# Performance work log

Hardware: AMD Instinct MI355X
Metric: run time of the kernel (lower is better)

The kernel has to match this reference:

```python
import jax, jax.numpy as jnp
import numpy as np

N = 8192
C = 256


def setup_inputs() -> dict:
    key = jax.random.key(0)
    k_x, k_wr, k_br, k_wc, k_bc = jax.random.split(key, 5)
    scale = 1.0 / np.sqrt(C)
    return {
        "x": jax.random.normal(k_x, (N, C), dtype=jnp.float32),
        "w_reduce": jax.random.uniform(k_wr, (C, C), dtype=jnp.float32, minval=-scale, maxval=scale),
        "b_reduce": jax.random.uniform(k_br, (C,), dtype=jnp.float32, minval=-scale, maxval=scale),
        "w_contr": jax.random.uniform(k_wc, (1, C), dtype=jnp.float32, minval=-scale, maxval=scale),
        "b_contr": jax.random.uniform(k_bc, (1,), dtype=jnp.float32, minval=-scale, maxval=scale),
    }


def reference(x, w_reduce, b_reduce, w_contr, b_contr):
    # Original math: y_ij = reduce(x_i + x_j); z_ij = sigmoid(contr(y_ij));
    # out_i = mean_j y_ij * z_ij.
    # Since reduce/contr are affine, decompose without the [N,N,C] tensor:
    #   y_ij = r_i + r_j + b_reduce,        r = x @ Wr^T
    #   contr(y_ij) = s_i + s_j + c0,       s = r . wc, c0 = b_reduce . wc + bc
    n = x.shape[0]
    r = x @ w_reduce.T                                   # [N, C]
    wc = w_contr[0]                                      # [C]
    s = r @ wc                                           # [N]
    c0 = b_reduce @ wc + b_contr[0]                      # scalar
    Z = jax.nn.sigmoid(s[:, None] + s[None, :] + c0)     # [N, N] pairwise gate
    m = jnp.mean(Z, axis=1, keepdims=True)               # [N, 1]
    # mean_j (r_i + r_j + b) * z_ij = (r_i + b) * m_i + (Z @ r)_i / N
    out = (r + b_reduce) * m + (Z @ r) / n               # [N, C]
    return out
```

## Files before the change

kernel.cpp:

```cpp
#include <hip/hip_runtime.h>
#include <hip/hip_bf16.h>
#include <stdint.h>

#define NN 8192
#define CC 256
#define NSPLIT 8
#define JR (NN / NSPLIT)
#define NITER (JR / 32)

typedef float f32x4 __attribute__((ext_vector_type(4)));
typedef float f32x2 __attribute__((ext_vector_type(2)));
typedef short s16x8 __attribute__((ext_vector_type(8)));

#define LOG2E 1.4426950408889634f

#define OFF_WT  0
#define OFF_R   (OFF_WT + CC*CC)
#define OFF_S2  (OFF_R + NN*CC)
#define OFF_C0  (OFF_S2 + NN)
#define OFF_SS  (OFF_C0 + 16)
#define OFF_SP  (OFF_SS + NSPLIT*NN)
#define OFF_V   (OFF_SP + 4*NN)
#define OFF_RB  (OFF_V + (NSPLIT*NN*CC)/2)

__global__ __launch_bounds__(256) void k_prep(const float* __restrict__ w,
                                              const float* __restrict__ br,
                                              const float* __restrict__ wcv,
                                              const float* __restrict__ bc,
                                              float* __restrict__ ws) {
  int k = blockIdx.x, c = threadIdx.x;
  ws[OFF_WT + k * CC + c] = w[c * CC + k];
  if (blockIdx.x == 0 && threadIdx.x < 64) {
    int lane = threadIdx.x;
    f32x4 b4 = *(const f32x4*)&br[lane * 4];
    f32x4 w4 = *(const f32x4*)&wcv[lane * 4];
    float d = b4[0]*w4[0] + b4[1]*w4[1] + b4[2]*w4[2] + b4[3]*w4[3];
    #pragma unroll
    for (int m = 32; m >= 1; m >>= 1) d += __shfl_xor(d, m, 64);
    if (lane == 0) { ws[OFF_C0] = d + bc[0]; ws[OFF_C0 + 1] = (d + bc[0]) * LOG2E; }
  }
}

__global__ __launch_bounds__(256) void k_r(const float* __restrict__ x,
                                           const float* __restrict__ wcv,
                                           float* __restrict__ ws) {
  __shared__ float xs[64][260];
  int bi = blockIdx.x;
  int rowblk = bi >> 2, colblk = bi & 3;
  int tid = threadIdx.x;
  int i0 = rowblk * 64;
  for (int t = tid; t < 64 * 64; t += 256) {
    int rr = t >> 6, c4 = t & 63;
    *(f32x4*)&xs[rr][c4 * 4] = *(const f32x4*)&x[(i0 + rr) * CC + c4 * 4];
  }
  __syncthreads();
  int tx = tid & 15, ty = tid >> 4;
  int cbase = colblk * 64 + tx * 4;
  int r0 = ty * 4;
  float acc[4][4] = {};
  const float* wt = ws + OFF_WT;
  for (int k = 0; k < CC; k += 2) {
    f32x4 wv0 = *(const f32x4*)&wt[k * CC + cbase];
    f32x4 wv1 = *(const f32x4*)&wt[(k + 1) * CC + cbase];
    f32x2 xv[4];
    #pragma unroll
    for (int rr = 0; rr < 4; rr++) xv[rr] = *(const f32x2*)&xs[r0 + rr][k];
    #pragma unroll
    for (int rr = 0; rr < 4; rr++)
      #pragma unroll
      for (int cc = 0; cc < 4; cc++)
        acc[rr][cc] = fmaf(xv[rr][1], wv1[cc], fmaf(xv[rr][0], wv0[cc], acc[rr][cc]));
  }
  #pragma unroll
  for (int rr = 0; rr < 4; rr++) {
    f32x4 o = {acc[rr][0], acc[rr][1], acc[rr][2], acc[rr][3]};
    *(f32x4*)&ws[OFF_R + (size_t)(i0 + r0 + rr) * CC + cbase] = o;
  }
  unsigned long long* rb64 = (unsigned long long*)(ws + OFF_RB);
  int j0r = i0 + r0;
  #pragma unroll
  for (int cc = 0; cc < 4; cc++) {
    int c = cbase + cc;
    unsigned long long v = 0;
    #pragma unroll
    for (int rr = 0; rr < 4; rr++) {
      unsigned u = __float_as_uint(acc[rr][cc]);
      u = (u + 0x7fffu + ((u >> 16) & 1u)) >> 16;
      v |= (unsigned long long)u << (16 * rr);
    }
    int us = (((j0r >> 5) * 16 + (c >> 4)) * 64 + (((j0r >> 3) & 3) * 16 + (c & 15))) * 8 + (j0r & 7);
    rb64[us >> 2] = v;
  }
  f32x4 wc4 = *(const f32x4*)&wcv[cbase];
  float sd[4];
  #pragma unroll
  for (int rr = 0; rr < 4; rr++) {
    sd[rr] = acc[rr][0]*wc4[0] + acc[rr][1]*wc4[1] + acc[rr][2]*wc4[2] + acc[rr][3]*wc4[3];
    #pragma unroll
    for (int m = 1; m < 16; m <<= 1) sd[rr] += __shfl_xor(sd[rr], m, 64);
  }
  if (tx == 0) {
    #pragma unroll
    for (int rr = 0; rr < 4; rr++)
      ws[OFF_SP + colblk * NN + j0r + rr] = sd[rr];
  }
}

__global__ __launch_bounds__(256) void k_s2(float* __restrict__ ws) {
  int row = blockIdx.x * 256 + threadIdx.x;
  float s = ws[OFF_SP + row] + ws[OFF_SP + NN + row]
          + ws[OFF_SP + 2 * NN + row] + ws[OFF_SP + 3 * NN + row];
  ws[OFF_S2 + row] = s * LOG2E;
}


#define STAGE(BUF, IT) { \
  const char* gb_ = rbase + (size_t)(IT) * 16384 + w * 1024 + l * 16; \
  _Pragma("unroll") \
  for (int q_ = 0; q_ < 4; q_++) \
    __builtin_amdgcn_global_load_lds( \
      (const __attribute__((address_space(1))) void*)(gb_ + q_ * 4096), \
      (__attribute__((address_space(3))) void*)&ldsb[(BUF) * 16384 + w * 1024 + q_ * 4096], \
      16, 0, 0); }

#define WAITBAR4 { asm volatile("s_waitcnt vmcnt(4)" ::: "memory"); \
  __builtin_amdgcn_s_barrier(); \
  __builtin_amdgcn_sched_barrier(0); }

#define WAITBAR0 { asm volatile("s_waitcnt vmcnt(0)" ::: "memory"); \
  __builtin_amdgcn_s_barrier(); \
  __builtin_amdgcn_sched_barrier(0); }

#define SB0 __builtin_amdgcn_sched_barrier(0);

#define SIGMOID(IT, AFA, AFB) { \
  f32x4 sj0_ = *(const f32x4*)&s2l[(IT) * 32 + g * 8]; \
  f32x4 sj1_ = *(const f32x4*)&s2l[(IT) * 32 + g * 8 + 4]; \
  _Pragma("unroll") \
  for (int t_ = 0; t_ < 8; t_++) { \
    float sj_ = (t_ < 4) ? sj0_[t_] : sj1_[t_ - 4]; \
    float eA_, eB_; \
    asm("v_exp_f32 %0, %1" : "=v"(eA_) : "v"(negaA - sj_)); \
    asm("v_exp_f32 %0, %1" : "=v"(eB_) : "v"(negaB - sj_)); \
    float zA_ = __builtin_amdgcn_rcpf(1.0f + eA_); \
    float zB_ = __builtin_amdgcn_rcpf(1.0f + eB_); \
    (AFA)[t_] = (short)(__float_as_uint(zA_) >> 16); \
    (AFB)[t_] = (short)(__float_as_uint(zB_) >> 16); } }

#define BLOAD(BF, LP) { \
  _Pragma("unroll") \
  for (int ct_ = 0; ct_ < 16; ct_++) \
    BF[ct_] = *(const s16x8*)((LP) + ct_ * 1024 + l * 16); }

#define MFMA_APPLY(AFA, AFB, BF) { \
  _Pragma("unroll") \
  for (int ct_ = 0; ct_ < 16; ct_++) { \
    accA[ct_] = __builtin_amdgcn_mfma_f32_16x16x32_bf16(AFA, BF[ct_], accA[ct_], 0, 0, 0); \
    accB[ct_] = __builtin_amdgcn_mfma_f32_16x16x32_bf16(AFB, BF[ct_], accB[ct_], 0, 0, 0); } \
  acc1A = __builtin_amdgcn_mfma_f32_16x16x32_bf16(AFA, ones, acc1A, 0, 0, 0); \
  acc1B = __builtin_amdgcn_mfma_f32_16x16x32_bf16(AFB, ones, acc1B, 0, 0, 0); }

__global__ __launch_bounds__(256, 2) void k_main(float* __restrict__ ws) {
  __shared__ char ldsb[3 * 16384];
  __shared__ float s2l[1024];
  int blk = blockIdx.x;
  int rt = blk >> 3, h = blk & 7;
  int tid = threadIdx.x;
  int w = tid >> 6, l = tid & 63;
  int lr = l & 15, g = l >> 4;
  int iw = rt * 128 + w * 32;
  float c02 = ws[OFF_C0 + 1];
  float negaA = -(ws[OFF_S2 + iw + lr] + c02);
  float negaB = -(ws[OFF_S2 + iw + 16 + lr] + c02);

  const float* s2p = ws + OFF_S2 + h * JR;
  *(f32x4*)&s2l[tid * 4] = *(const f32x4*)(s2p + tid * 4);
  __syncthreads();

  f32x4 accA[16], accB[16], acc1A, acc1B;
  #pragma unroll
  for (int i = 0; i < 16; i++) { accA[i] = (f32x4)(0.f); accB[i] = (f32x4)(0.f); }
  acc1A = (f32x4)(0.f); acc1B = (f32x4)(0.f);
  s16x8 ones;
  #pragma unroll
  for (int t = 0; t < 8; t++) ones[t] = (short)0x3F80;

  const char* rbase = (const char*)(ws + OFF_RB) + (size_t)h * (JR * CC * 2);

  STAGE(0, 0);
  STAGE(1, 1);
  s16x8 afA0, afB0, afA1, afB1;
  s16x8 bf[16];
  SIGMOID(0, afA0, afB0);

  int sA = 0;
  #pragma unroll 1
  for (int J = 0; J < NITER - 2; J += 2) {
    int sB = sA + 1; if (sB == 3) sB = 0;
    int sC = sB + 1; if (sC == 3) sC = 0;

    WAITBAR4;
    STAGE(sC, J + 2);
    SB0;
    BLOAD(bf, ldsb + sA * 16384);
    SB0;
    SIGMOID(J + 1, afA1, afB1);
    MFMA_APPLY(afA0, afB0, bf);

    WAITBAR4;
    STAGE(sA, J + 3);
    SB0;
    BLOAD(bf, ldsb + sB * 16384);
    SB0;
    SIGMOID(J + 2, afA0, afB0);
    MFMA_APPLY(afA1, afB1, bf);

    sA = sC;
  }
  {
    int sB = sA + 1; if (sB == 3) sB = 0;
    WAITBAR4;
    BLOAD(bf, ldsb + sA * 16384);
    SB0;
    SIGMOID(NITER - 1, afA1, afB1);
    MFMA_APPLY(afA0, afB0, bf);
    WAITBAR0;
    BLOAD(bf, ldsb + sB * 16384);
    MFMA_APPLY(afA1, afB1, bf);
  }

  if (lr == 0) {
    #pragma unroll
    for (int q = 0; q < 4; q++) {
      ws[OFF_SS + h * NN + iw + g * 4 + q] = acc1A[q];
      ws[OFF_SS + h * NN + iw + 16 + g * 4 + q] = acc1B[q];
    }
  }
  unsigned short* Vb = (unsigned short*)(ws + OFF_V);
  size_t vbase = (size_t)h * (NN * CC);
  #pragma unroll
  for (int ct = 0; ct < 16; ct++) {
    #pragma unroll
    for (int q = 0; q < 4; q++) {
      unsigned uA = __float_as_uint(accA[ct][q]);
      uA = (uA + 0x7fffu + ((uA >> 16) & 1u)) >> 16;
      Vb[vbase + (size_t)(iw + g * 4 + q) * CC + ct * 16 + lr] = (unsigned short)uA;
      unsigned uB = __float_as_uint(accB[ct][q]);
      uB = (uB + 0x7fffu + ((uB >> 16) & 1u)) >> 16;
      Vb[vbase + (size_t)(iw + 16 + g * 4 + q) * CC + ct * 16 + lr] = (unsigned short)uB;
    }
  }
}

__global__ __launch_bounds__(256) void k_epi(const float* __restrict__ br,
                                             const float* __restrict__ ws,
                                             float* __restrict__ out) {
  int idx = blockIdx.x * 256 + threadIdx.x;
  int i = idx >> 5, c8 = (idx & 31) * 8;
  float S = 0.f;
  #pragma unroll
  for (int p = 0; p < NSPLIT; p++) S += ws[OFF_SS + p * NN + i];
  float m = S * (1.0f / NN);
  float v[8] = {};
  const unsigned short* Vb = (const unsigned short*)(ws + OFF_V);
  #pragma unroll
  for (int p = 0; p < NSPLIT; p++) {
    s16x8 pv = *(const s16x8*)&Vb[(size_t)p * (NN * CC) + (size_t)i * CC + c8];
    #pragma unroll
    for (int t = 0; t < 8; t++)
      v[t] += __uint_as_float(((unsigned)(unsigned short)pv[t]) << 16);
  }
  f32x4 r0 = *(const f32x4*)&ws[OFF_R + (size_t)i * CC + c8];
  f32x4 r1 = *(const f32x4*)&ws[OFF_R + (size_t)i * CC + c8 + 4];
  f32x4 b0 = *(const f32x4*)&br[c8];
  f32x4 b1 = *(const f32x4*)&br[c8 + 4];
  f32x4 o0, o1;
  #pragma unroll
  for (int t = 0; t < 4; t++) {
    o0[t] = (r0[t] + b0[t]) * m + v[t] * (1.0f / NN);
    o1[t] = (r1[t] + b1[t]) * m + v[t + 4] * (1.0f / NN);
  }
  *(f32x4*)&out[(size_t)i * CC + c8] = o0;
  *(f32x4*)&out[(size_t)i * CC + c8 + 4] = o1;
}

extern "C" void kernel_launch(void* const* d_in, const int* in_sizes, int n_in,
                              void* d_out, int out_size, void* d_ws, size_t ws_size,
                              hipStream_t stream) {
  const float* x  = (const float*)d_in[0];
  const float* w  = (const float*)d_in[1];
  const float* br = (const float*)d_in[2];
  const float* wc = (const float*)d_in[3];
  const float* bc = (const float*)d_in[4];
  float* ws = (float*)d_ws;
  float* out = (float*)d_out;
  (void)in_sizes; (void)n_in; (void)out_size; (void)ws_size;

  k_prep<<<256, 256, 0, stream>>>(w, br, wc, bc, ws);
  k_r<<<512, 256, 0, stream>>>(x, wc, ws);
  k_s2<<<32, 256, 0, stream>>>(ws);
  k_main<<<512, 256, 0, stream>>>(ws);
  k_epi<<<1024, 256, 0, stream>>>(br, ws, out);
}
```

Baseline: 84.64 us.

## Switch pairwise gate GEMM from bf16 to fp8 MFMA with fp8-packed operands

```diff
diff --git a/kernel.cpp b/kernel.cpp
--- a/kernel.cpp
+++ b/kernel.cpp
@@ -76,20 +76,16 @@
     f32x4 o = {acc[rr][0], acc[rr][1], acc[rr][2], acc[rr][3]};
     *(f32x4*)&ws[OFF_R + (size_t)(i0 + r0 + rr) * CC + cbase] = o;
   }
-  unsigned long long* rb64 = (unsigned long long*)(ws + OFF_RB);
+  unsigned* rb32 = (unsigned*)(ws + OFF_RB);
   int j0r = i0 + r0;
   #pragma unroll
   for (int cc = 0; cc < 4; cc++) {
     int c = cbase + cc;
-    unsigned long long v = 0;
-    #pragma unroll
-    for (int rr = 0; rr < 4; rr++) {
-      unsigned u = __float_as_uint(acc[rr][cc]);
-      u = (u + 0x7fffu + ((u >> 16) & 1u)) >> 16;
-      v |= (unsigned long long)u << (16 * rr);
-    }
+    unsigned pk = 0;
+    pk = __builtin_amdgcn_cvt_pk_fp8_f32(acc[0][cc], acc[1][cc], (int)pk, false);
+    pk = __builtin_amdgcn_cvt_pk_fp8_f32(acc[2][cc], acc[3][cc], (int)pk, true);
     int us = (((j0r >> 5) * 16 + (c >> 4)) * 64 + (((j0r >> 3) & 3) * 16 + (c & 15))) * 8 + (j0r & 7);
-    rb64[us >> 2] = v;
+    rb32[us >> 2] = pk;
   }
   f32x4 wc4 = *(const f32x4*)&wcv[cbase];
   float sd[4];
@@ -115,15 +111,15 @@
 
 
 #define STAGE(BUF, IT) { \
-  const char* gb_ = rbase + (size_t)(IT) * 16384 + w * 1024 + l * 16; \
+  const char* gb_ = rbase + (size_t)(IT) * 8192 + w * 1024 + l * 16; \
   _Pragma("unroll") \
-  for (int q_ = 0; q_ < 4; q_++) \
+  for (int q_ = 0; q_ < 2; q_++) \
     __builtin_amdgcn_global_load_lds( \
       (const __attribute__((address_space(1))) void*)(gb_ + q_ * 4096), \
-      (__attribute__((address_space(3))) void*)&ldsb[(BUF) * 16384 + w * 1024 + q_ * 4096], \
+      (__attribute__((address_space(3))) void*)&ldsb[(BUF) * 8192 + w * 1024 + q_ * 4096], \
       16, 0, 0); }
 
-#define WAITBAR4 { asm volatile("s_waitcnt vmcnt(4)" ::: "memory"); \
+#define WAITBAR2 { asm volatile("s_waitcnt vmcnt(2)" ::: "memory"); \
   __builtin_amdgcn_s_barrier(); \
   __builtin_amdgcn_sched_barrier(0); }
 
@@ -136,32 +132,42 @@
 #define SIGMOID(IT, AFA, AFB) { \
   f32x4 sj0_ = *(const f32x4*)&s2l[(IT) * 32 + g * 8]; \
   f32x4 sj1_ = *(const f32x4*)&s2l[(IT) * 32 + g * 8 + 4]; \
+  float zA_[8], zB_[8]; \
   _Pragma("unroll") \
   for (int t_ = 0; t_ < 8; t_++) { \
     float sj_ = (t_ < 4) ? sj0_[t_] : sj1_[t_ - 4]; \
     float eA_, eB_; \
     asm("v_exp_f32 %0, %1" : "=v"(eA_) : "v"(negaA - sj_)); \
     asm("v_exp_f32 %0, %1" : "=v"(eB_) : "v"(negaB - sj_)); \
-    float zA_ = __builtin_amdgcn_rcpf(1.0f + eA_); \
-    float zB_ = __builtin_amdgcn_rcpf(1.0f + eB_); \
-    (AFA)[t_] = (short)(__float_as_uint(zA_) >> 16); \
-    (AFB)[t_] = (short)(__float_as_uint(zB_) >> 16); } }
+    zA_[t_] = __builtin_amdgcn_rcpf(1.0f + eA_); \
+    zB_[t_] = __builtin_amdgcn_rcpf(1.0f + eB_); } \
+  unsigned loA_ = 0, hiA_ = 0, loB_ = 0, hiB_ = 0; \
+  loA_ = __builtin_amdgcn_cvt_pk_fp8_f32(zA_[0], zA_[1], (int)loA_, false); \
+  loA_ = __builtin_amdgcn_cvt_pk_fp8_f32(zA_[2], zA_[3], (int)loA_, true); \
+  hiA_ = __builtin_amdgcn_cvt_pk_fp8_f32(zA_[4], zA_[5], (int)hiA_, false); \
+  hiA_ = __builtin_amdgcn_cvt_pk_fp8_f32(zA_[6], zA_[7], (int)hiA_, true); \
+  loB_ = __builtin_amdgcn_cvt_pk_fp8_f32(zB_[0], zB_[1], (int)loB_, false); \
+  loB_ = __builtin_amdgcn_cvt_pk_fp8_f32(zB_[2], zB_[3], (int)loB_, true); \
+  hiB_ = __builtin_amdgcn_cvt_pk_fp8_f32(zB_[4], zB_[5], (int)hiB_, false); \
+  hiB_ = __builtin_amdgcn_cvt_pk_fp8_f32(zB_[6], zB_[7], (int)hiB_, true); \
+  AFA = (long)(((unsigned long long)hiA_ << 32) | loA_); \
+  AFB = (long)(((unsigned long long)hiB_ << 32) | loB_); }
 
 #define BLOAD(BF, LP) { \
   _Pragma("unroll") \
   for (int ct_ = 0; ct_ < 16; ct_++) \
-    BF[ct_] = *(const s16x8*)((LP) + ct_ * 1024 + l * 16); }
+    BF[ct_] = *(const long*)((LP) + ct_ * 512 + l * 8); }
 
 #define MFMA_APPLY(AFA, AFB, BF) { \
   _Pragma("unroll") \
   for (int ct_ = 0; ct_ < 16; ct_++) { \
-    accA[ct_] = __builtin_amdgcn_mfma_f32_16x16x32_bf16(AFA, BF[ct_], accA[ct_], 0, 0, 0); \
-    accB[ct_] = __builtin_amdgcn_mfma_f32_16x16x32_bf16(AFB, BF[ct_], accB[ct_], 0, 0, 0); } \
-  acc1A = __builtin_amdgcn_mfma_f32_16x16x32_bf16(AFA, ones, acc1A, 0, 0, 0); \
-  acc1B = __builtin_amdgcn_mfma_f32_16x16x32_bf16(AFB, ones, acc1B, 0, 0, 0); }
+    accA[ct_] = __builtin_amdgcn_mfma_f32_16x16x32_fp8_fp8(AFA, BF[ct_], accA[ct_], 0, 0, 0); \
+    accB[ct_] = __builtin_amdgcn_mfma_f32_16x16x32_fp8_fp8(AFB, BF[ct_], accB[ct_], 0, 0, 0); } \
+  acc1A = __builtin_amdgcn_mfma_f32_16x16x32_fp8_fp8(AFA, ones, acc1A, 0, 0, 0); \
+  acc1B = __builtin_amdgcn_mfma_f32_16x16x32_fp8_fp8(AFB, ones, acc1B, 0, 0, 0); }
 
 __global__ __launch_bounds__(256, 2) void k_main(float* __restrict__ ws) {
-  __shared__ char ldsb[3 * 16384];
+  __shared__ char ldsb[3 * 8192];
   __shared__ float s2l[1024];
   int blk = blockIdx.x;
   int rt = blk >> 3, h = blk & 7;
@@ -181,16 +187,14 @@
   #pragma unroll
   for (int i = 0; i < 16; i++) { accA[i] = (f32x4)(0.f); accB[i] = (f32x4)(0.f); }
   acc1A = (f32x4)(0.f); acc1B = (f32x4)(0.f);
-  s16x8 ones;
-  #pragma unroll
-  for (int t = 0; t < 8; t++) ones[t] = (short)0x3F80;
-
-  const char* rbase = (const char*)(ws + OFF_RB) + (size_t)h * (JR * CC * 2);
+  const long ones = 0x3838383838383838LL;
+
+  const char* rbase = (const char*)(ws + OFF_RB) + (size_t)h * (JR * CC);
 
   STAGE(0, 0);
   STAGE(1, 1);
-  s16x8 afA0, afB0, afA1, afB1;
-  s16x8 bf[16];
+  long afA0, afB0, afA1, afB1;
+  long bf[16];
   SIGMOID(0, afA0, afB0);
 
   int sA = 0;
@@ -199,18 +203,18 @@
     int sB = sA + 1; if (sB == 3) sB = 0;
     int sC = sB + 1; if (sC == 3) sC = 0;
 
-    WAITBAR4;
+    WAITBAR2;
     STAGE(sC, J + 2);
     SB0;
-    BLOAD(bf, ldsb + sA * 16384);
+    BLOAD(bf, ldsb + sA * 8192);
     SB0;
     SIGMOID(J + 1, afA1, afB1);
     MFMA_APPLY(afA0, afB0, bf);
 
-    WAITBAR4;
+    WAITBAR2;
     STAGE(sA, J + 3);
     SB0;
-    BLOAD(bf, ldsb + sB * 16384);
+    BLOAD(bf, ldsb + sB * 8192);
     SB0;
     SIGMOID(J + 2, afA0, afB0);
     MFMA_APPLY(afA1, afB1, bf);
@@ -219,13 +223,13 @@
   }
   {
     int sB = sA + 1; if (sB == 3) sB = 0;
-    WAITBAR4;
-    BLOAD(bf, ldsb + sA * 16384);
+    WAITBAR2;
+    BLOAD(bf, ldsb + sA * 8192);
     SB0;
     SIGMOID(NITER - 1, afA1, afB1);
     MFMA_APPLY(afA0, afB0, bf);
     WAITBAR0;
-    BLOAD(bf, ldsb + sB * 16384);
+    BLOAD(bf, ldsb + sB * 8192);
     MFMA_APPLY(afA1, afB1, bf);
   }
 
```

Result: faster. 80.20 us (-5.2%).
